# Optimization experiments

Hardware: AMD Instinct MI355X
Metric: run time of the kernel (lower is better)

## Reference

```python
import jax, jax.numpy as jnp
import numpy as np

T, B, DIN, DLAT = 512, 128, 256, 512

def setup_inputs() -> dict:
    key = jax.random.key(0)
    k1, k2, k3, k4, k5 = jax.random.split(key, 5)
    s_i = 1.0 / np.sqrt(DIN)
    s_h = 1.0 / np.sqrt(DLAT)
    return {
        "X": jax.random.normal(k1, (T, B, DIN), dtype=jnp.float32),
        "h": jnp.zeros((B, DLAT), dtype=jnp.float32),
        "Wi": jax.random.uniform(k2, (DLAT, DIN), jnp.float32, -s_i, s_i),
        "bi": jax.random.uniform(k3, (DLAT,), jnp.float32, -s_i, s_i),
        "Wh": jax.random.uniform(k4, (DLAT, DLAT), jnp.float32, -s_h, s_h),
        "bh": jax.random.uniform(k5, (DLAT,), jnp.float32, -s_h, s_h),
    }

def reference(X, h, Wi, bi, Wh, bh):
    # Precompute input projection for all timesteps at once: [T,B,DLAT]
    Xi = jnp.einsum('tbd,ld->tbl', X, Wi) + bi + bh
    def step(h_prev, xi_t):
        h_t = jnp.tanh(xi_t + h_prev @ Wh.T)  # [B, DLAT]
        return h_t, h_t
    _, H = jax.lax.scan(step, h, Xi)
    return H  # [T, B, DLAT]
```

## Files before the change

kernel.cpp:

```cpp
#include <hip/hip_runtime.h>

#define T_STEPS 512
#define BATCH   128
#define DIN     256
#define DLAT    512

typedef __bf16 bf16x8 __attribute__((ext_vector_type(8)));
typedef float  f32x4  __attribute__((ext_vector_type(4)));
typedef int    i32x4  __attribute__((ext_vector_type(4)));
typedef unsigned long long u64;

__device__ __forceinline__ unsigned int f2bf2(float a, float b) {
  unsigned int ua = __float_as_uint(a);
  unsigned int ub = __float_as_uint(b);
  ua = (ua + 0x7FFFu + ((ua >> 16) & 1u)) >> 16;
  ub = (ub + 0x7FFFu + ((ub >> 16) & 1u)) >> 16;
  return ua | (ub << 16);
}

__device__ __forceinline__ uint4 pack8(float4 f0, float4 f1) {
  uint4 r;
  r.x = f2bf2(f0.x, f0.y);
  r.y = f2bf2(f0.z, f0.w);
  r.z = f2bf2(f1.x, f1.y);
  r.w = f2bf2(f1.z, f1.w);
  return r;
}

extern "C" __global__ __launch_bounds__(256) void pk_wh(
    const float* __restrict__ Wh, unsigned int* __restrict__ out) {
  int idx = blockIdx.x * 256 + threadIdx.x;
  const float* src = Wh + (long)idx * 8;
  float4 f0 = *(const float4*)src;
  float4 f1 = *(const float4*)(src + 4);
  uint4 v = pack8(f0, f1);
  *(uint4*)(out + (long)idx * 4) = v;
}

extern "C" __global__ __launch_bounds__(256) void xi_gemm(
    const float* __restrict__ X, const float* __restrict__ Wi,
    const float* __restrict__ bi, const float* __restrict__ bh,
    float* __restrict__ XiOut) {
  extern __shared__ char smem[];
  char*  sX    = smem;
  char*  sW    = smem + 65536;
  float* sBias = (float*)(smem + 131072);

  const int tid = threadIdx.x;
  const long m0 = (long)blockIdx.x * 128;
  const int  n0 = blockIdx.y * 128;

  #pragma unroll
  for (int c = 0; c < 16; ++c) {
    int id = c * 256 + tid;
    int r  = id >> 5;
    int kc = (id & 31) << 3;
    const float* sx = X + (m0 + r) * DIN + kc;
    float4 a0 = *(const float4*)sx;
    float4 a1 = *(const float4*)(sx + 4);
    int ax = ((r << 9) + (kc << 1)) ^ ((r & 7) << 4);
    *(uint4*)(sX + ax) = pack8(a0, a1);
    const float* sw = Wi + (n0 + r) * DIN + kc;
    float4 b0 = *(const float4*)sw;
    float4 b1 = *(const float4*)(sw + 4);
    *(uint4*)(sW + ax) = pack8(b0, b1);
  }
  if (tid < 128) sBias[tid] = bi[n0 + tid] + bh[n0 + tid];
  __syncthreads();

  const int w = tid >> 6, lane = tid & 63;
  const int wm = (w >> 1) * 64, wn = (w & 1) * 64;
  const int lm = lane & 15, lq = lane >> 4;

  f32x4 acc[4][4];
  #pragma unroll
  for (int nt = 0; nt < 4; ++nt) {
    float bv = sBias[wn + nt * 16 + lm];
    #pragma unroll
    for (int mt = 0; mt < 4; ++mt) acc[mt][nt] = f32x4{bv, bv, bv, bv};
  }

  #pragma unroll
  for (int k0 = 0; k0 < 8; ++k0) {
    int kb = (k0 << 6) + (lq << 4);
    bf16x8 af[4], bfr[4];
    #pragma unroll
    for (int mt = 0; mt < 4; ++mt) {
      int row = wm + mt * 16 + lm;
      int ax = ((row << 9) + kb) ^ ((row & 7) << 4);
      af[mt] = __builtin_bit_cast(bf16x8, *(uint4*)(sX + ax));
    }
    #pragma unroll
    for (int nt = 0; nt < 4; ++nt) {
      int row = wn + nt * 16 + lm;
      int ax = ((row << 9) + kb) ^ ((row & 7) << 4);
      bfr[nt] = __builtin_bit_cast(bf16x8, *(uint4*)(sW + ax));
    }
    #pragma unroll
    for (int mt = 0; mt < 4; ++mt)
      #pragma unroll
      for (int nt = 0; nt < 4; ++nt)
        acc[mt][nt] = __builtin_amdgcn_mfma_f32_16x16x32_bf16(af[mt], bfr[nt], acc[mt][nt], 0, 0, 0);
  }

  #pragma unroll
  for (int mt = 0; mt < 4; ++mt) {
    #pragma unroll
    for (int e = 0; e < 4; ++e) {
      long m = m0 + wm + mt * 16 + (lq << 2) + e;
      float* dst = XiOut + m * DLAT + n0 + wn + lm;
      #pragma unroll
      for (int nt = 0; nt < 4; ++nt)
        dst[nt * 16] = acc[mt][nt][e];
    }
  }
}

extern "C" __global__ __launch_bounds__(512, 2) void rnn_scan(
    const float* __restrict__ h0, const unsigned short* __restrict__ WhP,
    float* __restrict__ HO, u64* __restrict__ hx,
    unsigned int* __restrict__ flags) {
  __shared__ uint4 sH4[1024];
  char* sH = (char*)sH4;

  const int tid = threadIdx.x;
  const int w = tid >> 6, lane = tid & 63;
  const int lm = lane & 15, lq = lane >> 4;
  const int g  = blockIdx.x & 7;
  const int q  = blockIdx.x >> 3;
  const int r0 = g << 4;
  const int nt = (q << 7) + (w << 4);

  i32x4 wreg[16];
  {
    const unsigned short* base = WhP + (nt + lm) * DLAT + (lq << 3);
    #pragma unroll
    for (int kq = 0; kq < 16; ++kq)
      wreg[kq] = *(const i32x4*)(base + kq * 32);
    #pragma unroll
    for (int kq = 0; kq < 16; ++kq)
      asm("" : "+v"(wreg[kq]));
  }

  #pragma unroll
  for (int c = 0; c < 2; ++c) {
    int id = c * 512 + tid;
    int m = id >> 6, kc = (id & 63) << 3;
    const float* src = h0 + (r0 + m) * DLAT + kc;
    float4 f0 = *(const float4*)src;
    float4 f1 = *(const float4*)(src + 4);
    int ax = ((m << 10) + (kc << 1)) ^ ((m & 7) << 4);
    *(uint4*)(sH + ax) = pack8(f0, f1);
  }
  __syncthreads();

  const int mask  = (lm & 7) << 4;
  const int hbase = (lm << 10) + (lq << 4);
  const int ncol  = nt + (lq << 2);
  unsigned int* fgrp = flags + (g << 11);
  const int sq = (q + 1 + lane) & 3;
  const int rm = tid >> 5, rj = tid & 31;
  const int q1 = (q + 1) & 3, q2 = (q + 2) & 3, q3 = (q + 3) & 3;

  float4 xi = *(const float4*)(HO + (long)(r0 + lm) * DLAT + ncol);

  for (int t = 0; t < T_STEPS; ++t) {
    f32x4 a0 = f32x4{0.f, 0.f, 0.f, 0.f};
    f32x4 a1 = f32x4{0.f, 0.f, 0.f, 0.f};
    f32x4 a2 = f32x4{0.f, 0.f, 0.f, 0.f};
    f32x4 a3 = f32x4{0.f, 0.f, 0.f, 0.f};
    #pragma unroll
    for (int kq = 0; kq < 16; kq += 4) {
      bf16x8 hb0 = __builtin_bit_cast(bf16x8, *(uint4*)(sH + ((hbase + kq * 64) ^ mask)));
      bf16x8 hb1 = __builtin_bit_cast(bf16x8, *(uint4*)(sH + ((hbase + (kq + 1) * 64) ^ mask)));
      bf16x8 hb2 = __builtin_bit_cast(bf16x8, *(uint4*)(sH + ((hbase + (kq + 2) * 64) ^ mask)));
      bf16x8 hb3 = __builtin_bit_cast(bf16x8, *(uint4*)(sH + ((hbase + (kq + 3) * 64) ^ mask)));
      a0 = __builtin_amdgcn_mfma_f32_16x16x32_bf16(
          __builtin_bit_cast(bf16x8, wreg[kq]), hb0, a0, 0, 0, 0);
      a1 = __builtin_amdgcn_mfma_f32_16x16x32_bf16(
          __builtin_bit_cast(bf16x8, wreg[kq + 1]), hb1, a1, 0, 0, 0);
      a2 = __builtin_amdgcn_mfma_f32_16x16x32_bf16(
          __builtin_bit_cast(bf16x8, wreg[kq + 2]), hb2, a2, 0, 0, 0);
      a3 = __builtin_amdgcn_mfma_f32_16x16x32_bf16(
          __builtin_bit_cast(bf16x8, wreg[kq + 3]), hb3, a3, 0, 0, 0);
    }

    float hv[4];
    #pragma unroll
    for (int e = 0; e < 4; ++e) {
      float z = (a0[e] + a1[e]) + (a2[e] + a3[e]) + ((float*)&xi)[e];
      float ex = __expf(2.0f * z);
      hv[e] = 1.0f - 2.0f / (ex + 1.0f);
    }

    if (t + 1 < T_STEPS) {
      u64* hxg = hx + ((long)(t & 1) << 14) + ((long)g << 11);
      u64 v = ((u64)f2bf2(hv[2], hv[3]) << 32) | (u64)f2bf2(hv[0], hv[1]);

      __hip_atomic_store(&hxg[(lm << 7) + (ncol >> 2)], v,
                         __ATOMIC_RELAXED, __HIP_MEMORY_SCOPE_AGENT);
      asm volatile("s_waitcnt vmcnt(0)" ::: "memory");
      __syncthreads();

      if (tid == 0)
        __hip_atomic_store(&fgrp[(q << 9) + t], 1u,
                           __ATOMIC_RELAXED, __HIP_MEMORY_SCOPE_AGENT);

      {
        int ax = ((lm << 10) + (ncol << 1)) ^ mask;
        *(u64*)(sH + ax) = v;
        float4 o; o.x = hv[0]; o.y = hv[1]; o.z = hv[2]; o.w = hv[3];
        *(float4*)(HO + ((long)t * BATCH + r0 + lm) * DLAT + ncol) = o;
        xi = *(const float4*)(HO + ((long)(t + 1) * BATCH + r0 + lm) * DLAT + ncol);
      }

      u64 d1, d2, d3;
      for (;;) {
        d1 = __hip_atomic_load(&hxg[(rm << 7) + (q1 << 5) + rj],
                               __ATOMIC_RELAXED, __HIP_MEMORY_SCOPE_AGENT);
        d2 = __hip_atomic_load(&hxg[(rm << 7) + (q2 << 5) + rj],
                               __ATOMIC_RELAXED, __HIP_MEMORY_SCOPE_AGENT);
        d3 = __hip_atomic_load(&hxg[(rm << 7) + (q3 << 5) + rj],
                               __ATOMIC_RELAXED, __HIP_MEMORY_SCOPE_AGENT);
        unsigned int fv = (lane < 3)
            ? __hip_atomic_load(&fgrp[(sq << 9) + t], __ATOMIC_RELAXED, __HIP_MEMORY_SCOPE_AGENT)
            : 1u;
        if (!__any(fv == 0u)) break;
      }
      asm volatile("" ::: "memory");

      {
        int ax1 = ((rm << 10) + (((q1 << 5) + rj) << 3)) ^ ((rm & 7) << 4);
        int ax2 = ((rm << 10) + (((q2 << 5) + rj) << 3)) ^ ((rm & 7) << 4);
        int ax3 = ((rm << 10) + (((q3 << 5) + rj) << 3)) ^ ((rm & 7) << 4);
        *(u64*)(sH + ax1) = d1;
        *(u64*)(sH + ax2) = d2;
        *(u64*)(sH + ax3) = d3;
      }

      __syncthreads();
    } else {
      float4 o; o.x = hv[0]; o.y = hv[1]; o.z = hv[2]; o.w = hv[3];
      *(float4*)(HO + ((long)t * BATCH + r0 + lm) * DLAT + ncol) = o;
    }
  }
}

extern "C" void kernel_launch(void* const* d_in, const int* in_sizes, int n_in,
                              void* d_out, int out_size, void* d_ws, size_t ws_size,
                              hipStream_t stream) {
  const float* X  = (const float*)d_in[0];
  const float* h0 = (const float*)d_in[1];
  const float* Wi = (const float*)d_in[2];
  const float* bi = (const float*)d_in[3];
  const float* Wh = (const float*)d_in[4];
  const float* bh = (const float*)d_in[5];
  float* out = (float*)d_out;

  unsigned int* whp   = (unsigned int*)d_ws;
  u64*          hx    = (u64*)((char*)d_ws + 524288);
  unsigned int* flags = (unsigned int*)((char*)d_ws + 786432);

  hipMemsetAsync(flags, 0, 65536, stream);

  hipFuncSetAttribute((const void*)xi_gemm, hipFuncAttributeMaxDynamicSharedMemorySize, 131584);

  pk_wh<<<128, 256, 0, stream>>>(Wh, whp);
  xi_gemm<<<dim3(512, 4), 256, 131584, stream>>>(X, Wi, bi, bh, out);
  rnn_scan<<<32, 512, 0, stream>>>(h0, (const unsigned short*)whp, out, hx, flags);
}
```

Measured before the change: 1.163 ms.

## Use per-wave monotonic flags and double-buffered LDS to drop a barrier per step

Each wave now publishes its own step counter after its global store, replacing the per-step flag array and the block-wide barrier that previously preceded a single thread's flag store. Consumers poll 24 per-wave flags and compare against the step number. The LDS hidden-state buffer is double-buffered, so writes for the next step do not race with reads of the current one. This removes one __syncthreads per timestep on the serial critical path, at the cost of polling more flag words and doubling the LDS footprint.

New measurement: 1.863 ms. 60.3% more time.

```diff
diff --git a/kernel.cpp b/kernel.cpp
--- a/kernel.cpp
+++ b/kernel.cpp
@@ -120,8 +120,8 @@
     const float* __restrict__ h0, const unsigned short* __restrict__ WhP,
     float* __restrict__ HO, u64* __restrict__ hx,
     unsigned int* __restrict__ flags) {
-  __shared__ uint4 sH4[1024];
-  char* sH = (char*)sH4;
+  __shared__ uint4 sHbuf[2048];
+  char* sB = (char*)sHbuf;
 
   const int tid = threadIdx.x;
   const int w = tid >> 6, lane = tid & 63;
@@ -150,31 +150,41 @@
     float4 f0 = *(const float4*)src;
     float4 f1 = *(const float4*)(src + 4);
     int ax = ((m << 10) + (kc << 1)) ^ ((m & 7) << 4);
-    *(uint4*)(sH + ax) = pack8(f0, f1);
+    *(uint4*)(sB + ax) = pack8(f0, f1);
   }
   __syncthreads();
 
   const int mask  = (lm & 7) << 4;
   const int hbase = (lm << 10) + (lq << 4);
   const int ncol  = nt + (lq << 2);
-  unsigned int* fgrp = flags + (g << 11);
-  const int sq = (q + 1 + lane) & 3;
+  u64* hgrp = hx + ((long)g << 11);
+  const int pubi = (lm << 7) + (ncol >> 2);
   const int rm = tid >> 5, rj = tid & 31;
   const int q1 = (q + 1) & 3, q2 = (q + 2) & 3, q3 = (q + 3) & 3;
+  const int i1 = (rm << 7) + (q1 << 5) + rj;
+  const int i2 = (rm << 7) + (q2 << 5) + rj;
+  const int i3 = (rm << 7) + (q3 << 5) + rj;
+
+  unsigned int* fgrp = flags + (g << 5);
+  unsigned int* myflag = fgrp + (q << 3) + w;
+  unsigned int* pollflag = fgrp + ((((q + 1 + (lane >> 3)) & 3) << 3) + (lane & 7));
 
   float4 xi = *(const float4*)(HO + (long)(r0 + lm) * DLAT + ncol);
 
   for (int t = 0; t < T_STEPS; ++t) {
+    char* cur = sB + ((t & 1) << 14);
+    char* nxt = sB + (((t + 1) & 1) << 14);
+
     f32x4 a0 = f32x4{0.f, 0.f, 0.f, 0.f};
     f32x4 a1 = f32x4{0.f, 0.f, 0.f, 0.f};
     f32x4 a2 = f32x4{0.f, 0.f, 0.f, 0.f};
     f32x4 a3 = f32x4{0.f, 0.f, 0.f, 0.f};
     #pragma unroll
     for (int kq = 0; kq < 16; kq += 4) {
-      bf16x8 hb0 = __builtin_bit_cast(bf16x8, *(uint4*)(sH + ((hbase + kq * 64) ^ mask)));
-      bf16x8 hb1 = __builtin_bit_cast(bf16x8, *(uint4*)(sH + ((hbase + (kq + 1) * 64) ^ mask)));
-      bf16x8 hb2 = __builtin_bit_cast(bf16x8, *(uint4*)(sH + ((hbase + (kq + 2) * 64) ^ mask)));
-      bf16x8 hb3 = __builtin_bit_cast(bf16x8, *(uint4*)(sH + ((hbase + (kq + 3) * 64) ^ mask)));
+      bf16x8 hb0 = __builtin_bit_cast(bf16x8, *(uint4*)(cur + ((hbase + kq * 64) ^ mask)));
+      bf16x8 hb1 = __builtin_bit_cast(bf16x8, *(uint4*)(cur + ((hbase + (kq + 1) * 64) ^ mask)));
+      bf16x8 hb2 = __builtin_bit_cast(bf16x8, *(uint4*)(cur + ((hbase + (kq + 2) * 64) ^ mask)));
+      bf16x8 hb3 = __builtin_bit_cast(bf16x8, *(uint4*)(cur + ((hbase + (kq + 3) * 64) ^ mask)));
       a0 = __builtin_amdgcn_mfma_f32_16x16x32_bf16(
           __builtin_bit_cast(bf16x8, wreg[kq]), hb0, a0, 0, 0, 0);
       a1 = __builtin_amdgcn_mfma_f32_16x16x32_bf16(
@@ -193,39 +203,39 @@
       hv[e] = 1.0f - 2.0f / (ex + 1.0f);
     }
 
+    unsigned int pr01 = f2bf2(hv[0], hv[1]);
+    unsigned int pr23 = f2bf2(hv[2], hv[3]);
+    u64 v = (u64)pr01 | ((u64)pr23 << 32);
+
     if (t + 1 < T_STEPS) {
-      u64* hxg = hx + ((long)(t & 1) << 14) + ((long)g << 11);
-      u64 v = ((u64)f2bf2(hv[2], hv[3]) << 32) | (u64)f2bf2(hv[0], hv[1]);
-
-      __hip_atomic_store(&hxg[(lm << 7) + (ncol >> 2)], v,
-                         __ATOMIC_RELAXED, __HIP_MEMORY_SCOPE_AGENT);
+      u64* hxg = hgrp + ((long)(t & 1) << 14);
+
+      __hip_atomic_store(&hxg[pubi], v, __ATOMIC_RELAXED, __HIP_MEMORY_SCOPE_AGENT);
       asm volatile("s_waitcnt vmcnt(0)" ::: "memory");
-      __syncthreads();
-
-      if (tid == 0)
-        __hip_atomic_store(&fgrp[(q << 9) + t], 1u,
+      if (lane == 0)
+        __hip_atomic_store(myflag, (unsigned int)(t + 1),
                            __ATOMIC_RELAXED, __HIP_MEMORY_SCOPE_AGENT);
 
       {
         int ax = ((lm << 10) + (ncol << 1)) ^ mask;
-        *(u64*)(sH + ax) = v;
+        *(u64*)(nxt + ax) = v;
         float4 o; o.x = hv[0]; o.y = hv[1]; o.z = hv[2]; o.w = hv[3];
         *(float4*)(HO + ((long)t * BATCH + r0 + lm) * DLAT + ncol) = o;
         xi = *(const float4*)(HO + ((long)(t + 1) * BATCH + r0 + lm) * DLAT + ncol);
       }
 
       u64 d1, d2, d3;
-      for (;;) {
-        d1 = __hip_atomic_load(&hxg[(rm << 7) + (q1 << 5) + rj],
-                               __ATOMIC_RELAXED, __HIP_MEMORY_SCOPE_AGENT);
-        d2 = __hip_atomic_load(&hxg[(rm << 7) + (q2 << 5) + rj],
-                               __ATOMIC_RELAXED, __HIP_MEMORY_SCOPE_AGENT);
-        d3 = __hip_atomic_load(&hxg[(rm << 7) + (q3 << 5) + rj],
-                               __ATOMIC_RELAXED, __HIP_MEMORY_SCOPE_AGENT);
-        unsigned int fv = (lane < 3)
-            ? __hip_atomic_load(&fgrp[(sq << 9) + t], __ATOMIC_RELAXED, __HIP_MEMORY_SCOPE_AGENT)
-            : 1u;
-        if (!__any(fv == 0u)) break;
+      {
+        const unsigned int want = (unsigned int)(t + 1);
+        for (;;) {
+          d1 = __hip_atomic_load(&hxg[i1], __ATOMIC_RELAXED, __HIP_MEMORY_SCOPE_AGENT);
+          d2 = __hip_atomic_load(&hxg[i2], __ATOMIC_RELAXED, __HIP_MEMORY_SCOPE_AGENT);
+          d3 = __hip_atomic_load(&hxg[i3], __ATOMIC_RELAXED, __HIP_MEMORY_SCOPE_AGENT);
+          unsigned int fv = (lane < 24)
+              ? __hip_atomic_load(pollflag, __ATOMIC_RELAXED, __HIP_MEMORY_SCOPE_AGENT)
+              : want;
+          if (!__any(fv < want)) break;
+        }
       }
       asm volatile("" ::: "memory");
 
@@ -233,9 +243,9 @@
         int ax1 = ((rm << 10) + (((q1 << 5) + rj) << 3)) ^ ((rm & 7) << 4);
         int ax2 = ((rm << 10) + (((q2 << 5) + rj) << 3)) ^ ((rm & 7) << 4);
         int ax3 = ((rm << 10) + (((q3 << 5) + rj) << 3)) ^ ((rm & 7) << 4);
-        *(u64*)(sH + ax1) = d1;
-        *(u64*)(sH + ax2) = d2;
-        *(u64*)(sH + ax3) = d3;
+        *(u64*)(nxt + ax1) = d1;
+        *(u64*)(nxt + ax2) = d2;
+        *(u64*)(nxt + ax3) = d3;
       }
 
       __syncthreads();
@@ -261,7 +271,7 @@
   u64*          hx    = (u64*)((char*)d_ws + 524288);
   unsigned int* flags = (unsigned int*)((char*)d_ws + 786432);
 
-  hipMemsetAsync(flags, 0, 65536, stream);
+  hipMemsetAsync(flags, 0, 1024, stream);
 
   hipFuncSetAttribute((const void*)xi_gemm, hipFuncAttributeMaxDynamicSharedMemorySize, 131584);
 
```
